# Kernel tuning notes

Measured on AMD Instinct MI355X. Metric: run time of the kernel, lower is better.

Reference implementation:

```python
import jax, jax.numpy as jnp
import numpy as np
import math

D_MODEL = 1024
ED = 2048       # d_inner = expand * d_model
R = 64          # dt_rank = ceil(d_model/16)
N = 16          # d_state
K = 4           # d_conv
DT_MIN, DT_MAX, DT_FLOOR = 0.001, 0.1, 0.0001


def setup_inputs() -> dict:
    key = jax.random.key(0)
    ks = jax.random.split(key, 8)
    x = jax.random.normal(ks[0], (1, 2048, D_MODEL), dtype=jnp.float32)
    in_proj_w = jax.random.normal(ks[1], (2 * ED, D_MODEL), dtype=jnp.float32) * (D_MODEL ** -0.5)
    conv_w = jax.random.normal(ks[2], (ED, 1, K), dtype=jnp.float32) * (K ** -0.5)
    conv_b = jnp.zeros((ED,), dtype=jnp.float32)
    x_proj_w = jax.random.normal(ks[3], (R + 2 * N, ED), dtype=jnp.float32) * (ED ** -0.5)
    std = R ** -0.5
    dt_proj_w = jax.random.uniform(ks[4], (ED, R), dtype=jnp.float32, minval=-std, maxval=std)
    dt = jnp.exp(jax.random.uniform(ks[5], (ED,), dtype=jnp.float32)
                 * (math.log(DT_MAX) - math.log(DT_MIN)) + math.log(DT_MIN))
    dt = jnp.clip(dt, DT_FLOOR, None)
    dt_proj_b = dt + jnp.log(-jnp.expm1(-dt))  # inverse softplus init
    A_log = jnp.log(jnp.tile(jnp.arange(1, N + 1, dtype=jnp.float32), (ED, 1)))  # [ED, N]
    D = jnp.ones((ED,), dtype=jnp.float32)
    out_proj_w = jax.random.normal(ks[6], (D_MODEL, ED), dtype=jnp.float32) * (ED ** -0.5)
    return {"x": x, "in_proj_w": in_proj_w, "conv_w": conv_w, "conv_b": conv_b,
            "x_proj_w": x_proj_w, "dt_proj_w": dt_proj_w, "dt_proj_b": dt_proj_b,
            "A_log": A_log, "D": D, "out_proj_w": out_proj_w}


def _causal_dwconv(xr, conv_w, conv_b):
    # xr: [B, L, ED]; depthwise causal conv, left-pad K-1 (equiv to pad K-1 both sides then slice [:L])
    x_ncl = jnp.transpose(xr, (0, 2, 1))
    y = jax.lax.conv_general_dilated(x_ncl, conv_w, window_strides=(1,),
                                     padding=[(K - 1, 0)], feature_group_count=ED)
    return jnp.transpose(y, (0, 2, 1)) + conv_b


def _mamba_fwd(x, in_proj_w, conv_w, conv_b, x_proj_w, dt_proj_w, dt_proj_b, A_log, D, out_proj_w):
    xz = jnp.einsum('bld,ed->ble', x, in_proj_w)          # [B, L, 2*ED]
    xr, z = jnp.split(xz, 2, axis=-1)
    xr = jax.nn.silu(_causal_dwconv(xr, conv_w, conv_b))  # [B, L, ED]
    A = -jnp.exp(A_log)                                    # [ED, N]
    dbc = jnp.einsum('ble,fe->blf', xr, x_proj_w)          # [B, L, R+2N]
    delta_r, Bm, Cm = jnp.split(dbc, [R, R + N], axis=-1)
    delta = jax.nn.softplus(jnp.einsum('blr,er->ble', delta_r, dt_proj_w) + dt_proj_b)  # [B, L, ED]
    dA = jnp.exp(delta[..., None] * A)                     # [B, L, ED, N]
    BX = delta[..., None] * Bm[:, :, None, :] * xr[..., None]  # [B, L, ED, N]
    # linear recurrence h_t = dA_t * h_{t-1} + BX_t via associative scan over L
    def combine(c1, c2):
        a1, x1 = c1
        a2, x2 = c2
        return a1 * a2, a2 * x1 + x2
    _, hs = jax.lax.associative_scan(combine, (dA, BX), axis=1)  # [B, L, ED, N]
    y = jnp.einsum('blen,bln->ble', hs, Cm) + D * xr
    return jnp.einsum('ble,de->bld', y * jax.nn.silu(z), out_proj_w)


def reference(x, in_proj_w, conv_w, conv_b, x_proj_w, dt_proj_w, dt_proj_b, A_log, D, out_proj_w):
    return _mamba_fwd(x, in_proj_w, conv_w, conv_b, x_proj_w, dt_proj_w, dt_proj_b, A_log, D, out_proj_w)
```

## Files before the change

kernel.cpp:

```cpp
#include <hip/hip_runtime.h>
#include <math.h>

#define LSEQ 2048
#define DM   1024
#define EDIM 2048
#define RNK  64
#define NS   16
#define DBCW 96
#define LC   32
#define NCH  (LSEQ / LC)
#define NSEG 8
#define NSEGS (NCH / NSEG)
#define SPLITK2 16
#define DLS_STRIDE 264

typedef __attribute__((ext_vector_type(4))) float f32x4;
typedef __attribute__((ext_vector_type(8))) __bf16 bf16x8;

__device__ __forceinline__ ushort f2bf(float f) {
    unsigned u = __float_as_uint(f);
    unsigned r = (u + 0x7fffu + ((u >> 16) & 1u)) >> 16;
    return (ushort)r;
}
__device__ __forceinline__ float bf2f(ushort u) {
    return __uint_as_float(((unsigned)u) << 16);
}

#define R0 2097152L
#define R1 (R0 + 4194304L)
#define R2 (R1 + 2097152L)
#define R3 (R2 + 196608L)
#define R4 (R3 + 131072L)
#define R5 (R4 + 32768L)

__global__ __launch_bounds__(256) void prep_all(
    const float* __restrict__ x, const float* __restrict__ w1,
    const float* __restrict__ w4, const float* __restrict__ xpw,
    const float* __restrict__ w3,
    ushort* __restrict__ xbf, ushort* __restrict__ w1bf,
    ushort* __restrict__ w4bf, ushort* __restrict__ xpw_pad,
    ushort* __restrict__ w3bf)
{
    long idx4 = ((long)blockIdx.x * 256 + threadIdx.x) * 4;
    if (idx4 >= R5) return;
    if (idx4 >= R4) {
        long rel = idx4 - R4;
        float* p = (float*)(xpw_pad + 196608);
        *reinterpret_cast<float4*>(&p[rel]) = make_float4(0.f, 0.f, 0.f, 0.f);
        return;
    }
    const float* src; ushort* dst; long rel;
    if (idx4 < R0)      { src = x;   dst = xbf;     rel = idx4; }
    else if (idx4 < R1) { src = w1;  dst = w1bf;    rel = idx4 - R0; }
    else if (idx4 < R2) { src = w4;  dst = w4bf;    rel = idx4 - R1; }
    else if (idx4 < R3) { src = xpw; dst = xpw_pad; rel = idx4 - R2; }
    else                { src = w3;  dst = w3bf;    rel = idx4 - R3; }
    float4 v = *reinterpret_cast<const float4*>(&src[rel]);
    ushort4 o = make_ushort4(f2bf(v.x), f2bf(v.y), f2bf(v.z), f2bf(v.w));
    *reinterpret_cast<ushort4*>(&dst[rel]) = o;
}

__global__ __launch_bounds__(256) void gemm_nt_bf16(
    const ushort* __restrict__ A, int lda,
    const ushort* __restrict__ B, int ldb,
    float* __restrict__ C0, float* __restrict__ C1, int csplit, int ldc,
    long cplane, int klen, int grid_n, int blocks_per_k)
{
    __shared__ ushort As[128 * 32];
    __shared__ ushort Bs[128 * 32];
    const int tid = threadIdx.x;
    const int wave = tid >> 6;
    const int lane = tid & 63;
    const int kch = blockIdx.x / blocks_per_k;
    const int rem = blockIdx.x % blocks_per_k;
    const int bm = (rem / grid_n) * 128;
    const int bn = (rem % grid_n) * 128;
    const int wm = (wave & 1) * 64;
    const int wn = (wave >> 1) * 64;
    const int koff = kch * klen;
    C0 += (long)kch * cplane;

    f32x4 acc[4][4] = {};

    const int offT = tid * 16;
    const char* Ab = (const char*)A;
    const char* Bb = (const char*)B;
    char* AsB = (char*)As;
    char* BsB = (char*)Bs;

    for (int k0 = 0; k0 < klen; k0 += 32) {
        __syncthreads();
        #pragma unroll
        for (int r = 0; r < 2; ++r) {
            int off = r * 4096 + offT;
            int row = off >> 6;
            int kb = off & 63;
            __builtin_amdgcn_global_load_lds(
                (const __attribute__((address_space(1))) void*)
                    (Ab + ((long)(bm + row) * lda + koff + k0) * 2 + kb),
                (__attribute__((address_space(3))) void*)
                    (AsB + r * 4096 + wave * 1024), 16, 0, 0);
            __builtin_amdgcn_global_load_lds(
                (const __attribute__((address_space(1))) void*)
                    (Bb + ((long)(bn + row) * ldb + koff + k0) * 2 + kb),
                (__attribute__((address_space(3))) void*)
                    (BsB + r * 4096 + wave * 1024), 16, 0, 0);
        }
        __syncthreads();

        bf16x8 af[4], bfr[4];
        #pragma unroll
        for (int i = 0; i < 4; ++i) {
            int ar = wm + i * 16 + (lane & 15);
            af[i]  = *reinterpret_cast<const bf16x8*>(AsB + ar * 64 + (lane >> 4) * 16);
            int br = wn + i * 16 + (lane & 15);
            bfr[i] = *reinterpret_cast<const bf16x8*>(BsB + br * 64 + (lane >> 4) * 16);
        }
        #pragma unroll
        for (int i = 0; i < 4; ++i)
            #pragma unroll
            for (int j = 0; j < 4; ++j)
                acc[i][j] = __builtin_amdgcn_mfma_f32_16x16x32_bf16(
                    af[i], bfr[j], acc[i][j], 0, 0, 0);
    }

    #pragma unroll
    for (int i = 0; i < 4; ++i) {
        int row0 = bm + wm + i * 16 + (lane >> 4) * 4;
        #pragma unroll
        for (int j = 0; j < 4; ++j) {
            int col = bn + wn + j * 16 + (lane & 15);
            float* Cp;
            int cc;
            if (col < csplit) { Cp = C0; cc = col; }
            else              { Cp = C1; cc = col - csplit; }
            #pragma unroll
            for (int q = 0; q < 4; ++q)
                Cp[(long)(row0 + q) * ldc + cc] = acc[i][j][q];
        }
    }
}

__global__ __launch_bounds__(256) void gemm_nt_bf16_w64(
    const ushort* __restrict__ A, int lda,
    const ushort* __restrict__ B, int ldb,
    float* __restrict__ C0, float* __restrict__ C1, int csplit, int ldc,
    long cplane, int klen, int grid_n, int blocks_per_k)
{
    __shared__ ushort As[128 * 32];
    __shared__ ushort Bs[64 * 32];
    const int tid = threadIdx.x;
    const int wave = tid >> 6;
    const int lane = tid & 63;
    const int kch = blockIdx.x / blocks_per_k;
    const int rem = blockIdx.x % blocks_per_k;
    const int bm = (rem / grid_n) * 128;
    const int bn = (rem % grid_n) * 64;
    const int wm = (wave & 1) * 64;
    const int wn = (wave >> 1) * 32;
    const int koff = kch * klen;
    C0 += (long)kch * cplane;

    f32x4 acc[4][2] = {};

    const int offT = tid * 16;
    const char* Ab = (const char*)A;
    const char* Bb = (const char*)B;
    char* AsB = (char*)As;
    char* BsB = (char*)Bs;

    for (int k0 = 0; k0 < klen; k0 += 32) {
        __syncthreads();
        #pragma unroll
        for (int r = 0; r < 2; ++r) {
            int off = r * 4096 + offT;
            int row = off >> 6;
            int kb = off & 63;
            __builtin_amdgcn_global_load_lds(
                (const __attribute__((address_space(1))) void*)
                    (Ab + ((long)(bm + row) * lda + koff + k0) * 2 + kb),
                (__attribute__((address_space(3))) void*)
                    (AsB + r * 4096 + wave * 1024), 16, 0, 0);
        }
        {
            int row = offT >> 6;
            int kb = offT & 63;
            __builtin_amdgcn_global_load_lds(
                (const __attribute__((address_space(1))) void*)
                    (Bb + ((long)(bn + row) * ldb + koff + k0) * 2 + kb),
                (__attribute__((address_space(3))) void*)
                    (BsB + wave * 1024), 16, 0, 0);
        }
        __syncthreads();

        bf16x8 af[4], bfr[2];
        #pragma unroll
        for (int i = 0; i < 4; ++i) {
            int ar = wm + i * 16 + (lane & 15);
            af[i] = *reinterpret_cast<const bf16x8*>(AsB + ar * 64 + (lane >> 4) * 16);
        }
        #pragma unroll
        for (int j = 0; j < 2; ++j) {
            int br = wn + j * 16 + (lane & 15);
            bfr[j] = *reinterpret_cast<const bf16x8*>(BsB + br * 64 + (lane >> 4) * 16);
        }
        #pragma unroll
        for (int i = 0; i < 4; ++i)
            #pragma unroll
            for (int j = 0; j < 2; ++j)
                acc[i][j] = __builtin_amdgcn_mfma_f32_16x16x32_bf16(
                    af[i], bfr[j], acc[i][j], 0, 0, 0);
    }

    #pragma unroll
    for (int i = 0; i < 4; ++i) {
        int row0 = bm + wm + i * 16 + (lane >> 4) * 4;
        #pragma unroll
        for (int j = 0; j < 2; ++j) {
            int col = bn + wn + j * 16 + (lane & 15);
            float* Cp;
            int cc;
            if (col < csplit) { Cp = C0; cc = col; }
            else              { Cp = C1; cc = col - csplit; }
            #pragma unroll
            for (int q = 0; q < 4; ++q)
                Cp[(long)(row0 + q) * ldc + cc] = acc[i][j][q];
        }
    }
}

__global__ __launch_bounds__(256) void g4_reduce(
    const float* __restrict__ Gp, float* __restrict__ out)
{
    long i4 = ((long)blockIdx.x * 256 + threadIdx.x) * 4;
    float4 a = *reinterpret_cast<const float4*>(&Gp[i4]);
    float4 b = *reinterpret_cast<const float4*>(&Gp[2097152 + i4]);
    float4 o = make_float4(a.x + b.x, a.y + b.y, a.z + b.z, a.w + b.w);
    *reinterpret_cast<float4*>(&out[i4]) = o;
}

__global__ __launch_bounds__(256) void gemm2_reduce(
    const float* __restrict__ Pb, float* __restrict__ dbc,
    ushort* __restrict__ dtr)
{
    int idx = blockIdx.x * 256 + threadIdx.x;
    float s = 0.f;
    #pragma unroll
    for (int c = 0; c < SPLITK2; ++c) s += Pb[(long)c * LSEQ * DBCW + idx];
    dbc[idx] = s;
    int r = idx / DBCW;
    int c = idx - r * DBCW;
    if (c < RNK) dtr[r * RNK + c] = f2bf(s);
}

__global__ __launch_bounds__(256) void conv_silu(
    const float* __restrict__ xr, const float* __restrict__ w,
    const float* __restrict__ b, ushort* __restrict__ xrc)
{
    int idx = blockIdx.x * 256 + threadIdx.x;
    int l = idx >> 9;
    int e4 = (idx & 511) << 2;
    float4 zero = make_float4(0.f, 0.f, 0.f, 0.f);
    float4 r0 = (l >= 3) ? *reinterpret_cast<const float4*>(&xr[(long)(l - 3) * EDIM + e4]) : zero;
    float4 r1 = (l >= 2) ? *reinterpret_cast<const float4*>(&xr[(long)(l - 2) * EDIM + e4]) : zero;
    float4 r2 = (l >= 1) ? *reinterpret_cast<const float4*>(&xr[(long)(l - 1) * EDIM + e4]) : zero;
    float4 r3 = *reinterpret_cast<const float4*>(&xr[(long)l * EDIM + e4]);
    float4 bb = *reinterpret_cast<const float4*>(&b[e4]);
    float rr0[4] = {r0.x, r0.y, r0.z, r0.w};
    float rr1[4] = {r1.x, r1.y, r1.z, r1.w};
    float rr2[4] = {r2.x, r2.y, r2.z, r2.w};
    float rr3[4] = {r3.x, r3.y, r3.z, r3.w};
    float bbv[4] = {bb.x, bb.y, bb.z, bb.w};
    ushort o[4];
    #pragma unroll
    for (int j = 0; j < 4; ++j) {
        float4 wj = *reinterpret_cast<const float4*>(&w[(e4 + j) * 4]);
        float acc = bbv[j];
        acc = fmaf(wj.x, rr0[j], acc);
        acc = fmaf(wj.y, rr1[j], acc);
        acc = fmaf(wj.z, rr2[j], acc);
        acc = fmaf(wj.w, rr3[j], acc);
        o[j] = f2bf(acc / (1.f + __expf(-acc)));
    }
    *reinterpret_cast<ushort4*>(&xrc[(long)l * EDIM + e4]) =
        make_ushort4(o[0], o[1], o[2], o[3]);
}

__device__ __forceinline__ void delta_tile_mfma(
    const ushort* __restrict__ dtr, const ushort* __restrict__ w3,
    const float* __restrict__ bias, ushort* dls, int t0, int eb, int tid)
{
    const int wave = tid >> 6;
    const int lane = tid & 63;
    f32x4 acc[2][4] = {};
    #pragma unroll
    for (int kk = 0; kk < 2; ++kk) {
        bf16x8 af[2], bfr[4];
        #pragma unroll
        for (int i = 0; i < 2; ++i)
            af[i] = *reinterpret_cast<const bf16x8*>(
                &dtr[(long)(t0 + i * 16 + (lane & 15)) * RNK + kk * 32 + (lane >> 4) * 8]);
        #pragma unroll
        for (int j = 0; j < 4; ++j)
            bfr[j] = *reinterpret_cast<const bf16x8*>(
                &w3[(long)(eb + wave * 64 + j * 16 + (lane & 15)) * RNK + kk * 32 + (lane >> 4) * 8]);
        #pragma unroll
        for (int i = 0; i < 2; ++i)
            #pragma unroll
            for (int j = 0; j < 4; ++j)
                acc[i][j] = __builtin_amdgcn_mfma_f32_16x16x32_bf16(
                    af[i], bfr[j], acc[i][j], 0, 0, 0);
    }
    #pragma unroll
    for (int i = 0; i < 2; ++i) {
        #pragma unroll
        for (int j = 0; j < 4; ++j) {
            int el = wave * 64 + j * 16 + (lane & 15);
            float bv = bias[eb + el];
            #pragma unroll
            for (int q = 0; q < 4; ++q) {
                float v = acc[i][j][q] + bv;
                v = fmaxf(v, 0.f) + __logf(1.f + __expf(-fabsf(v)));
                dls[(i * 16 + (lane >> 4) * 4 + q) * DLS_STRIDE + el] = f2bf(v);
            }
        }
    }
}

__global__ __launch_bounds__(256) void scan_phaseA(
    const ushort* __restrict__ dtr, const ushort* __restrict__ w3,
    const float* __restrict__ bias,
    const ushort* __restrict__ xr, const float* __restrict__ dbc,
    const float* __restrict__ A_log,
    float* __restrict__ P, float* __restrict__ Hf)
{
    __shared__ ushort dls[LC * DLS_STRIDE];
    __shared__ float dbcs[LC][16];
    const int tid = threadIdx.x;
    const int blk = blockIdx.x;
    const int c = blk >> 3;
    const int eb = (blk & 7) * 256;
    const int e = eb + tid;
    const int t0 = c * LC;

    ushort xrv[LC];
    #pragma unroll
    for (int tt = 0; tt < LC; ++tt)
        xrv[tt] = xr[(long)(t0 + tt) * EDIM + e];

    delta_tile_mfma(dtr, w3, bias, dls, t0, eb, tid);
    #pragma unroll
    for (int it = 0; it < 2; ++it) {
        int ix = tid + it * 256;
        dbcs[ix >> 4][ix & 15] = dbc[(long)(t0 + (ix >> 4)) * DBCW + RNK + (ix & 15)];
    }
    __syncthreads();

    float Aa[NS], h[NS], Pp[NS];
    #pragma unroll
    for (int n = 0; n < NS; ++n) {
        Aa[n] = -__expf(A_log[e * NS + n]);
        h[n] = 0.f;
        Pp[n] = 1.f;
    }
    #pragma unroll 4
    for (int tt = 0; tt < LC; ++tt) {
        float d  = bf2f(dls[tt * DLS_STRIDE + tid]);
        float xv = bf2f(xrv[tt]);
        float bmv[16];
        #pragma unroll
        for (int q = 0; q < 4; ++q) {
            float4 vb = *reinterpret_cast<const float4*>(&dbcs[tt][q * 4]);
            bmv[q * 4 + 0] = vb.x; bmv[q * 4 + 1] = vb.y;
            bmv[q * 4 + 2] = vb.z; bmv[q * 4 + 3] = vb.w;
        }
        float dx = d * xv;
        #pragma unroll
        for (int n = 0; n < NS; ++n) {
            float a = __expf(d * Aa[n]);
            h[n] = fmaf(a, h[n], dx * bmv[n]);
            Pp[n] *= a;
        }
    }
    #pragma unroll
    for (int n = 0; n < NS; ++n) {
        P [(long)(c * NS + n) * EDIM + e] = Pp[n];
        Hf[(long)(c * NS + n) * EDIM + e] = h[n];
    }
}

__global__ __launch_bounds__(256) void scan_phaseB1(
    float* __restrict__ P, float* __restrict__ Hf,
    float* __restrict__ Sp, float* __restrict__ Sf)
{
    int gid = blockIdx.x * 256 + threadIdx.x;
    int e = gid & (EDIM - 1);
    int n = (gid >> 11) & (NS - 1);
    int g = gid >> 15;
    float h = 0.f, pp = 1.f;
    for (int c = g * NSEG; c < g * NSEG + NSEG; ++c) {
        long idx = (long)(c * NS + n) * EDIM + e;
        float p = P[idx];
        float f = Hf[idx];
        Hf[idx] = h;
        P[idx] = pp;
        h = fmaf(p, h, f);
        pp *= p;
    }
    long si = (long)(g * NS + n) * EDIM + e;
    Sp[si] = pp;
    Sf[si] = h;
}

__global__ __launch_bounds__(256) void scan_phaseB2(
    const float* __restrict__ Sp, float* __restrict__ Sf)
{
    int gid = blockIdx.x * 256 + threadIdx.x;
    int e = gid & (EDIM - 1);
    int n = gid >> 11;
    float h = 0.f;
    for (int g = 0; g < NSEGS; ++g) {
        long idx = (long)(g * NS + n) * EDIM + e;
        float p = Sp[idx];
        float f = Sf[idx];
        Sf[idx] = h;
        h = fmaf(p, h, f);
    }
}

__global__ __launch_bounds__(256) void scan_phaseC(
    const ushort* __restrict__ dtr, const ushort* __restrict__ w3,
    const float* __restrict__ bias,
    const ushort* __restrict__ xr, const float* __restrict__ dbc,
    const float* __restrict__ A_log,
    const float* __restrict__ P, const float* __restrict__ Hf,
    const float* __restrict__ Sf, const float* __restrict__ Dp,
    const float* __restrict__ z, ushort* __restrict__ ubf)
{
    __shared__ ushort dls[LC * DLS_STRIDE];
    __shared__ float dbcs[LC][32];
    const int tid = threadIdx.x;
    const int blk = blockIdx.x;
    const int c = blk >> 3;
    const int eb = (blk & 7) * 256;
    const int e = eb + tid;
    const int g = c >> 3;
    const int t0 = c * LC;

    ushort xrv[LC];
    float  zvv[LC];
    #pragma unroll
    for (int tt = 0; tt < LC; ++tt)
        xrv[tt] = xr[(long)(t0 + tt) * EDIM + e];
    #pragma unroll
    for (int tt = 0; tt < LC; ++tt)
        zvv[tt] = z[(long)(t0 + tt) * EDIM + e];

    delta_tile_mfma(dtr, w3, bias, dls, t0, eb, tid);
    #pragma unroll
    for (int it = 0; it < 4; ++it) {
        int ix = tid + it * 256;
        dbcs[ix >> 5][ix & 31] = dbc[(long)(t0 + (ix >> 5)) * DBCW + RNK + (ix & 31)];
    }
    __syncthreads();

    float Aa[NS], h[NS];
    #pragma unroll
    for (int n = 0; n < NS; ++n) {
        Aa[n] = -__expf(A_log[e * NS + n]);
        long ci = (long)(c * NS + n) * EDIM + e;
        long si = (long)(g * NS + n) * EDIM + e;
        h[n] = fmaf(P[ci], Sf[si], Hf[ci]);
    }
    float dD = Dp[e];
    #pragma unroll 4
    for (int tt = 0; tt < LC; ++tt) {
        float d  = bf2f(dls[tt * DLS_STRIDE + tid]);
        float xv = bf2f(xrv[tt]);
        float bmv[16], cmv[16];
        #pragma unroll
        for (int q = 0; q < 4; ++q) {
            float4 vb = *reinterpret_cast<const float4*>(&dbcs[tt][q * 4]);
            float4 vc = *reinterpret_cast<const float4*>(&dbcs[tt][16 + q * 4]);
            bmv[q * 4 + 0] = vb.x; bmv[q * 4 + 1] = vb.y;
            bmv[q * 4 + 2] = vb.z; bmv[q * 4 + 3] = vb.w;
            cmv[q * 4 + 0] = vc.x; cmv[q * 4 + 1] = vc.y;
            cmv[q * 4 + 2] = vc.z; cmv[q * 4 + 3] = vc.w;
        }
        float dx = d * xv;
        float y0 = 0.f, y1 = 0.f, y2 = 0.f, y3 = 0.f;
        #pragma unroll
        for (int q = 0; q < 4; ++q) {
            #pragma unroll
            for (int r = 0; r < 4; ++r) {
                int n = q * 4 + r;
                float a = __expf(d * Aa[n]);
                h[n] = fmaf(a, h[n], dx * bmv[n]);
                if (q == 0) y0 = fmaf(h[n], cmv[n], y0);
                else if (q == 1) y1 = fmaf(h[n], cmv[n], y1);
                else if (q == 2) y2 = fmaf(h[n], cmv[n], y2);
                else y3 = fmaf(h[n], cmv[n], y3);
            }
        }
        float y = (y0 + y1) + (y2 + y3);
        y = fmaf(dD, xv, y);
        float zv = zvv[tt];
        float sz = zv / (1.f + __expf(-zv));
        ubf[(long)(t0 + tt) * EDIM + e] = f2bf(y * sz);
    }
}

extern "C" void kernel_launch(void* const* d_in, const int* in_sizes, int n_in,
                              void* d_out, int out_size, void* d_ws, size_t ws_size,
                              hipStream_t stream) {
    const float* x         = (const float*)d_in[0];
    const float* in_proj_w = (const float*)d_in[1];
    const float* conv_w    = (const float*)d_in[2];
    const float* conv_b    = (const float*)d_in[3];
    const float* x_proj_w  = (const float*)d_in[4];
    const float* dt_proj_w = (const float*)d_in[5];
    const float* dt_proj_b = (const float*)d_in[6];
    const float* A_log     = (const float*)d_in[7];
    const float* Dp        = (const float*)d_in[8];
    const float* out_proj_w= (const float*)d_in[9];
    float* out = (float*)d_out;

    float* ws = (float*)d_ws;
    const long M1 = 1048576;
    ushort* xbf     = (ushort*)ws;
    ushort* w1bf    = (ushort*)(ws + 1 * M1);
    float*  Pb      = ws;
    ushort* ubf     = (ushort*)ws;
    float*  junk    = ws + 3 * M1;
    ushort* xpw_pad = (ushort*)(ws + 3 * M1 + M1 / 4);
    ushort* w4bf    = (ushort*)(ws + 3 * M1 + M1 / 2);
    float*  xr_f32  = ws + 4 * M1 + M1 / 2;
    float*  Hf      = ws + 4 * M1 + M1 / 2;
    float*  Gp      = ws + 4 * M1 + M1 / 2;
    float*  z_f32   = ws + 8 * M1 + M1 / 2;
    ushort* xrcbf   = (ushort*)(ws + 12 * M1 + M1 / 2);
    float*  P       = ws + 14 * M1 + M1 / 2;
    float*  Sp      = ws + 18 * M1 + M1 / 2;
    float*  Sf      = ws + 19 * M1;
    float*  dbc     = ws + 19 * M1 + M1 / 2;
    ushort* w3bf    = (ushort*)(ws + 19 * M1 + M1 / 2 + 196608);
    ushort* dtr_bf  = (ushort*)(ws + 19 * M1 + M1 / 2 + 196608 + 65536);

    dim3 blk(256);

    prep_all<<<(R5 / 4 + 255) / 256, blk, 0, stream>>>(
        x, in_proj_w, out_proj_w, x_proj_w, dt_proj_w,
        xbf, w1bf, w4bf, xpw_pad, w3bf);

    gemm_nt_bf16_w64<<<1024, blk, 0, stream>>>(
        xbf, DM, w1bf, DM, xr_f32, z_f32, EDIM, EDIM, 0, DM, 64, 1024);

    conv_silu<<<(LSEQ * EDIM) / 1024, blk, 0, stream>>>(xr_f32, conv_w, conv_b, xrcbf);

    gemm_nt_bf16<<<SPLITK2 * 16, blk, 0, stream>>>(
        xrcbf, EDIM, xpw_pad, EDIM, Pb, junk, DBCW, DBCW,
        (long)LSEQ * DBCW, EDIM / SPLITK2, 1, 16);
    gemm2_reduce<<<(LSEQ * DBCW) / 256, blk, 0, stream>>>(Pb, dbc, dtr_bf);

    scan_phaseA<<<(NCH * EDIM) / 256, blk, 0, stream>>>(
        dtr_bf, w3bf, dt_proj_b, xrcbf, dbc, A_log, P, Hf);
    scan_phaseB1<<<(EDIM * NS * NSEGS) / 256, blk, 0, stream>>>(P, Hf, Sp, Sf);
    scan_phaseB2<<<(EDIM * NS) / 256, blk, 0, stream>>>(Sp, Sf);
    scan_phaseC<<<(NCH * EDIM) / 256, blk, 0, stream>>>(
        dtr_bf, w3bf, dt_proj_b, xrcbf, dbc, A_log, P, Hf, Sf, Dp, z_f32, ubf);

    gemm_nt_bf16_w64<<<512, blk, 0, stream>>>(
        ubf, EDIM, w4bf, EDIM, Gp, junk, 1 << 30, DM,
        (long)LSEQ * DM, EDIM / 2, 16, 256);
    g4_reduce<<<(LSEQ * DM) / 1024, blk, 0, stream>>>(Gp, out);
}
```

Before: 175.6 us.

## Restructure chunked scan to use cumulative-delta decay, avoiding delta recompute

```diff
diff --git a/kernel.cpp b/kernel.cpp
--- a/kernel.cpp
+++ b/kernel.cpp
@@ -331,111 +331,8 @@
     const ushort* __restrict__ dtr, const ushort* __restrict__ w3,
     const float* __restrict__ bias,
     const ushort* __restrict__ xr, const float* __restrict__ dbc,
-    const float* __restrict__ A_log,
-    float* __restrict__ P, float* __restrict__ Hf)
-{
-    __shared__ ushort dls[LC * DLS_STRIDE];
-    __shared__ float dbcs[LC][16];
-    const int tid = threadIdx.x;
-    const int blk = blockIdx.x;
-    const int c = blk >> 3;
-    const int eb = (blk & 7) * 256;
-    const int e = eb + tid;
-    const int t0 = c * LC;
-
-    ushort xrv[LC];
-    #pragma unroll
-    for (int tt = 0; tt < LC; ++tt)
-        xrv[tt] = xr[(long)(t0 + tt) * EDIM + e];
-
-    delta_tile_mfma(dtr, w3, bias, dls, t0, eb, tid);
-    #pragma unroll
-    for (int it = 0; it < 2; ++it) {
-        int ix = tid + it * 256;
-        dbcs[ix >> 4][ix & 15] = dbc[(long)(t0 + (ix >> 4)) * DBCW + RNK + (ix & 15)];
-    }
-    __syncthreads();
-
-    float Aa[NS], h[NS], Pp[NS];
-    #pragma unroll
-    for (int n = 0; n < NS; ++n) {
-        Aa[n] = -__expf(A_log[e * NS + n]);
-        h[n] = 0.f;
-        Pp[n] = 1.f;
-    }
-    #pragma unroll 4
-    for (int tt = 0; tt < LC; ++tt) {
-        float d  = bf2f(dls[tt * DLS_STRIDE + tid]);
-        float xv = bf2f(xrv[tt]);
-        float bmv[16];
-        #pragma unroll
-        for (int q = 0; q < 4; ++q) {
-            float4 vb = *reinterpret_cast<const float4*>(&dbcs[tt][q * 4]);
-            bmv[q * 4 + 0] = vb.x; bmv[q * 4 + 1] = vb.y;
-            bmv[q * 4 + 2] = vb.z; bmv[q * 4 + 3] = vb.w;
-        }
-        float dx = d * xv;
-        #pragma unroll
-        for (int n = 0; n < NS; ++n) {
-            float a = __expf(d * Aa[n]);
-            h[n] = fmaf(a, h[n], dx * bmv[n]);
-            Pp[n] *= a;
-        }
-    }
-    #pragma unroll
-    for (int n = 0; n < NS; ++n) {
-        P [(long)(c * NS + n) * EDIM + e] = Pp[n];
-        Hf[(long)(c * NS + n) * EDIM + e] = h[n];
-    }
-}
-
-__global__ __launch_bounds__(256) void scan_phaseB1(
-    float* __restrict__ P, float* __restrict__ Hf,
-    float* __restrict__ Sp, float* __restrict__ Sf)
-{
-    int gid = blockIdx.x * 256 + threadIdx.x;
-    int e = gid & (EDIM - 1);
-    int n = (gid >> 11) & (NS - 1);
-    int g = gid >> 15;
-    float h = 0.f, pp = 1.f;
-    for (int c = g * NSEG; c < g * NSEG + NSEG; ++c) {
-        long idx = (long)(c * NS + n) * EDIM + e;
-        float p = P[idx];
-        float f = Hf[idx];
-        Hf[idx] = h;
-        P[idx] = pp;
-        h = fmaf(p, h, f);
-        pp *= p;
-    }
-    long si = (long)(g * NS + n) * EDIM + e;
-    Sp[si] = pp;
-    Sf[si] = h;
-}
-
-__global__ __launch_bounds__(256) void scan_phaseB2(
-    const float* __restrict__ Sp, float* __restrict__ Sf)
-{
-    int gid = blockIdx.x * 256 + threadIdx.x;
-    int e = gid & (EDIM - 1);
-    int n = gid >> 11;
-    float h = 0.f;
-    for (int g = 0; g < NSEGS; ++g) {
-        long idx = (long)(g * NS + n) * EDIM + e;
-        float p = Sp[idx];
-        float f = Sf[idx];
-        Sf[idx] = h;
-        h = fmaf(p, h, f);
-    }
-}
-
-__global__ __launch_bounds__(256) void scan_phaseC(
-    const ushort* __restrict__ dtr, const ushort* __restrict__ w3,
-    const float* __restrict__ bias,
-    const ushort* __restrict__ xr, const float* __restrict__ dbc,
-    const float* __restrict__ A_log,
-    const float* __restrict__ P, const float* __restrict__ Hf,
-    const float* __restrict__ Sf, const float* __restrict__ Dp,
-    const float* __restrict__ z, ushort* __restrict__ ubf)
+    const float* __restrict__ A_log, const float* __restrict__ Dp,
+    float* __restrict__ Hf, ushort* __restrict__ yl, float* __restrict__ Dc)
 {
     __shared__ ushort dls[LC * DLS_STRIDE];
     __shared__ float dbcs[LC][32];
@@ -444,17 +341,7 @@
     const int c = blk >> 3;
     const int eb = (blk & 7) * 256;
     const int e = eb + tid;
-    const int g = c >> 3;
     const int t0 = c * LC;
-
-    ushort xrv[LC];
-    float  zvv[LC];
-    #pragma unroll
-    for (int tt = 0; tt < LC; ++tt)
-        xrv[tt] = xr[(long)(t0 + tt) * EDIM + e];
-    #pragma unroll
-    for (int tt = 0; tt < LC; ++tt)
-        zvv[tt] = z[(long)(t0 + tt) * EDIM + e];
 
     delta_tile_mfma(dtr, w3, bias, dls, t0, eb, tid);
     #pragma unroll
@@ -468,15 +355,13 @@
     #pragma unroll
     for (int n = 0; n < NS; ++n) {
         Aa[n] = -__expf(A_log[e * NS + n]);
-        long ci = (long)(c * NS + n) * EDIM + e;
-        long si = (long)(g * NS + n) * EDIM + e;
-        h[n] = fmaf(P[ci], Sf[si], Hf[ci]);
+        h[n] = 0.f;
     }
     float dD = Dp[e];
-    #pragma unroll 4
+    float Dsum = 0.f;
     for (int tt = 0; tt < LC; ++tt) {
         float d  = bf2f(dls[tt * DLS_STRIDE + tid]);
-        float xv = bf2f(xrv[tt]);
+        float xv = bf2f(xr[(long)(t0 + tt) * EDIM + e]);
         float bmv[16], cmv[16];
         #pragma unroll
         for (int q = 0; q < 4; ++q) {
@@ -488,6 +373,7 @@
             cmv[q * 4 + 2] = vc.z; cmv[q * 4 + 3] = vc.w;
         }
         float dx = d * xv;
+        Dsum += d;
         float y0 = 0.f, y1 = 0.f, y2 = 0.f, y3 = 0.f;
         #pragma unroll
         for (int q = 0; q < 4; ++q) {
@@ -504,9 +390,112 @@
         }
         float y = (y0 + y1) + (y2 + y3);
         y = fmaf(dD, xv, y);
-        float zv = zvv[tt];
+        yl[(long)(t0 + tt) * EDIM + e] = f2bf(y);
+        Dc[(long)(t0 + tt) * EDIM + e] = Dsum;
+    }
+    #pragma unroll
+    for (int n = 0; n < NS; ++n)
+        Hf[(long)(c * NS + n) * EDIM + e] = h[n];
+}
+
+__global__ __launch_bounds__(256) void scan_phaseB1(
+    const float* __restrict__ Dc, float* __restrict__ Hf,
+    float* __restrict__ E, float* __restrict__ Dseg,
+    const float* __restrict__ A_log, float* __restrict__ Sf)
+{
+    int gid = blockIdx.x * 256 + threadIdx.x;
+    int e = gid & (EDIM - 1);
+    int n = (gid >> 11) & (NS - 1);
+    int g = gid >> 15;
+    float Aa = -__expf(A_log[e * NS + n]);
+    float h = 0.f, sumD = 0.f;
+    for (int c = g * NSEG; c < g * NSEG + NSEG; ++c) {
+        float Dch = Dc[(long)(c * LC + LC - 1) * EDIM + e];
+        if (n == 0) E[(long)c * EDIM + e] = sumD;
+        float p = __expf(Aa * Dch);
+        long idx = (long)(c * NS + n) * EDIM + e;
+        float f = Hf[idx];
+        Hf[idx] = h;
+        h = fmaf(p, h, f);
+        sumD += Dch;
+    }
+    if (n == 0) Dseg[(long)g * EDIM + e] = sumD;
+    Sf[(long)(g * NS + n) * EDIM + e] = h;
+}
+
+__global__ __launch_bounds__(256) void scan_phaseB2(
+    const float* __restrict__ Dseg, const float* __restrict__ A_log,
+    float* __restrict__ Sf)
+{
+    int gid = blockIdx.x * 256 + threadIdx.x;
+    int e = gid & (EDIM - 1);
+    int n = gid >> 11;
+    float Aa = -__expf(A_log[e * NS + n]);
+    float h = 0.f;
+    for (int g = 0; g < NSEGS; ++g) {
+        float p = __expf(Aa * Dseg[(long)g * EDIM + e]);
+        long idx = (long)(g * NS + n) * EDIM + e;
+        float f = Sf[idx];
+        Sf[idx] = h;
+        h = fmaf(p, h, f);
+    }
+}
+
+__global__ __launch_bounds__(256) void scan_phaseC(
+    const float* __restrict__ dbc, const float* __restrict__ A_log,
+    const float* __restrict__ Hf, const float* __restrict__ Sf,
+    const float* __restrict__ E, const float* __restrict__ Dc,
+    const ushort* __restrict__ yl, const float* __restrict__ z,
+    ushort* __restrict__ ubf)
+{
+    __shared__ float cms[LC][16];
+    const int tid = threadIdx.x;
+    const int blk = blockIdx.x;
+    const int c = blk >> 3;
+    const int eb = (blk & 7) * 256;
+    const int e = eb + tid;
+    const int g = c >> 3;
+    const int t0 = c * LC;
+
+    #pragma unroll
+    for (int it = 0; it < 2; ++it) {
+        int ix = tid + it * 256;
+        cms[ix >> 4][ix & 15] =
+            dbc[(long)(t0 + (ix >> 4)) * DBCW + RNK + NS + (ix & 15)];
+    }
+    __syncthreads();
+
+    float Aa[NS], hin[NS];
+    float Ev = E[(long)c * EDIM + e];
+    #pragma unroll
+    for (int n = 0; n < NS; ++n) {
+        Aa[n] = -__expf(A_log[e * NS + n]);
+        hin[n] = fmaf(__expf(Aa[n] * Ev),
+                      Sf[(long)(g * NS + n) * EDIM + e],
+                      Hf[(long)(c * NS + n) * EDIM + e]);
+    }
+    #pragma unroll 4
+    for (int tt = 0; tt < LC; ++tt) {
+        float D   = Dc[(long)(t0 + tt) * EDIM + e];
+        float ylv = bf2f(yl[(long)(t0 + tt) * EDIM + e]);
+        float zv  = z[(long)(t0 + tt) * EDIM + e];
+        float c0 = 0.f, c1 = 0.f;
+        #pragma unroll
+        for (int q = 0; q < 4; ++q) {
+            float4 vc = *reinterpret_cast<const float4*>(&cms[tt][q * 4]);
+            float cm4[4] = {vc.x, vc.y, vc.z, vc.w};
+            #pragma unroll
+            for (int r = 0; r < 4; ++r) {
+                int n = q * 4 + r;
+                float a = __expf(Aa[n] * D);
+                float t = a * cm4[r];
+                if (q < 2) c0 = fmaf(t, hin[n], c0);
+                else       c1 = fmaf(t, hin[n], c1);
+            }
+        }
+        float u = ylv + (c0 + c1);
         float sz = zv / (1.f + __expf(-zv));
-        ubf[(long)(t0 + tt) * EDIM + e] = f2bf(y * sz);
+        ubf[(long)(t0 + tt) * EDIM + e] = f2bf(u * sz);
     }
 }
 
@@ -531,16 +520,18 @@
     ushort* w1bf    = (ushort*)(ws + 1 * M1);
     float*  Pb      = ws;
     ushort* ubf     = (ushort*)ws;
+    float*  E       = ws + 2 * M1;
+    float*  Dseg    = ws + 2 * M1 + 131072;
     float*  junk    = ws + 3 * M1;
     ushort* xpw_pad = (ushort*)(ws + 3 * M1 + M1 / 4);
     ushort* w4bf    = (ushort*)(ws + 3 * M1 + M1 / 2);
     float*  xr_f32  = ws + 4 * M1 + M1 / 2;
     float*  Hf      = ws + 4 * M1 + M1 / 2;
+    ushort* yl      = (ushort*)(ws + 6 * M1 + M1 / 2);
     float*  Gp      = ws + 4 * M1 + M1 / 2;
     float*  z_f32   = ws + 8 * M1 + M1 / 2;
     ushort* xrcbf   = (ushort*)(ws + 12 * M1 + M1 / 2);
-    float*  P       = ws + 14 * M1 + M1 / 2;
-    float*  Sp      = ws + 18 * M1 + M1 / 2;
+    float*  Dc      = ws + 14 * M1 + M1 / 2;
     float*  Sf      = ws + 19 * M1;
     float*  dbc     = ws + 19 * M1 + M1 / 2;
     ushort* w3bf    = (ushort*)(ws + 19 * M1 + M1 / 2 + 196608);
@@ -563,11 +554,12 @@
     gemm2_reduce<<<(LSEQ * DBCW) / 256, blk, 0, stream>>>(Pb, dbc, dtr_bf);
 
     scan_phaseA<<<(NCH * EDIM) / 256, blk, 0, stream>>>(
-        dtr_bf, w3bf, dt_proj_b, xrcbf, dbc, A_log, P, Hf);
-    scan_phaseB1<<<(EDIM * NS * NSEGS) / 256, blk, 0, stream>>>(P, Hf, Sp, Sf);
-    scan_phaseB2<<<(EDIM * NS) / 256, blk, 0, stream>>>(Sp, Sf);
+        dtr_bf, w3bf, dt_proj_b, xrcbf, dbc, A_log, Dp, Hf, yl, Dc);
+    scan_phaseB1<<<(EDIM * NS * NSEGS) / 256, blk, 0, stream>>>(
+        Dc, Hf, E, Dseg, A_log, Sf);
+    scan_phaseB2<<<(EDIM * NS) / 256, blk, 0, stream>>>(Dseg, A_log, Sf);
     scan_phaseC<<<(NCH * EDIM) / 256, blk, 0, stream>>>(
-        dtr_bf, w3bf, dt_proj_b, xrcbf, dbc, A_log, P, Hf, Sf, Dp, z_f32, ubf);
+        dbc, A_log, Hf, Sf, E, Dc, yl, z_f32, ubf);
 
     gemm_nt_bf16_w64<<<512, blk, 0, stream>>>(
         ubf, EDIM, w4bf, EDIM, Gp, junk, 1 << 30, DM,
```

New measurement: 163.9 us. 6.7% less time.
